# Optimization experiments

Measured on AMD Instinct MI355X. Metric: run time of the kernel, lower is better.

The kernel has to match this reference:

```python
import jax, jax.numpy as jnp
from jax import lax
import numpy as np

B = 512

def setup_inputs() -> dict:
    key = jax.random.key(0)
    ks = jax.random.split(key, 6)
    x = jax.random.normal(ks[0], (B, 1, 28, 28), jnp.float32)
    conv1_w = jax.random.normal(ks[1], (256, 1, 9, 9), jnp.float32) * 0.05
    conv1_b = jnp.zeros((256,), jnp.float32)
    prim_w = jax.random.normal(ks[2], (32, 32, 1, 9, 9), jnp.float32) * 0.02
    prim_b = jnp.zeros((32,), jnp.float32)
    dig_W = jax.random.normal(ks[3], (1152, 8, 16), jnp.float32) * 0.1
    dig_Wb = jnp.zeros((1152, 16), jnp.float32)
    out_w = jax.random.normal(ks[4], (10, 10, 16, 1), jnp.float32) * 0.1
    out_b = jnp.zeros((10,), jnp.float32)
    return dict(x=x, conv1_w=conv1_w, conv1_b=conv1_b, prim_w=prim_w, prim_b=prim_b,
                dig_W=dig_W, dig_Wb=dig_Wb, out_w=out_w, out_b=out_b)


def _squash(s):
    # s: [B, 16, 10]; matches torch: v = ||s||_2/(1+||s||_2) * (s^T / ||s||_1)
    l2 = jnp.sqrt(jnp.sum(s * s, axis=1))[:, :, None]      # [B, 10, 1]
    l1 = jnp.sum(jnp.abs(s), axis=1)[:, :, None]            # [B, 10, 1]
    return l2 / (1.0 + l2) * (jnp.swapaxes(s, 1, 2) / l1)   # [B, 10, 16]


def reference(x, conv1_w, conv1_b, prim_w, prim_b, dig_W, dig_Wb, out_w, out_b):
    # conv1: [B,1,28,28] -> [B,256,20,20]
    out = lax.conv_general_dilated(x, conv1_w, (1, 1), 'VALID',
                                   dimension_numbers=('NCHW', 'OIHW', 'NCHW'))
    out = jax.nn.relu(out + conv1_b[None, :, None, None])
    # primary capsules: [B,32,8,20,20] -> [B,32,8,6,6]
    out1 = out.reshape(-1, 32, 8, 20, 20)
    out1 = lax.conv_general_dilated(out1, prim_w, (1, 2, 2), 'VALID',
                                    dimension_numbers=('NCDHW', 'OIDHW', 'NCDHW'))
    out1 = jax.nn.relu(out1 + prim_b[None, :, None, None, None])
    # transpose(2,-1) then reshape -> [B, 1152, 8]
    u = jnp.swapaxes(out1, 2, 4).reshape(-1, 1152, 8)
    # per-capsule affine: [B,1152,16]
    dig = jnp.einsum('bnd,nde->bne', u, dig_W) + dig_Wb
    bsz = dig.shape[0]
    # dynamic routing: b logits are never updated in the source, so
    # c = softmax(zeros, dim=1) = 1/1152 uniform, and all 3 iterations produce
    # the identical v. Computed once (same math as the original loop).
    c = jnp.full((bsz, 1152, 10), 1.0 / 1152, dtype=dig.dtype)
    s = jnp.einsum('bni,bnd->bdi', c, dig)   # [B, 16, 10]
    v = _squash(s)                            # [B, 10, 16]
    # output Conv2d(10,10,[16,1]) on v[...,None] reduces fully -> [B,10]
    logits = jnp.einsum('bik,oik->bo', v, out_w[..., 0]) + out_b
    return jax.nn.softmax(logits, axis=1)
```

## Files before the change

### kernel.cpp

```cpp
#include <hip/hip_runtime.h>
#include <math.h>


typedef __attribute__((ext_vector_type(8))) short bf16x8;
typedef __attribute__((ext_vector_type(4))) float f32x4;

__device__ inline unsigned short f2bf(float f) {
    union { float f; unsigned u; } v; v.f = f;
    unsigned r = v.u + 0x7fff + ((v.u >> 16) & 1);
    return (unsigned short)(r >> 16);
}

#define C1TN 16008

__global__ void caps_pre(const float* __restrict__ conv1_w,
                         const float* __restrict__ prim_w,
                         const float* __restrict__ dig_Wb,
                         const float* __restrict__ out_w,
                         float* __restrict__ S,
                         float* __restrict__ colsum,
                         float* __restrict__ OW,
                         unsigned short* __restrict__ c1wp2,
                         unsigned short* __restrict__ pw2,
                         unsigned int* __restrict__ cnt,
                         int B)
{
    const int t = threadIdx.x;
    const int bx = blockIdx.x;

    if (bx < 32) {
        __shared__ float lw[2592];
        const float* src = prim_w + bx * 32 * 81;
        for (int j = t; j < 2592; j += 256) lw[j] = src[j];
        __syncthreads();
        unsigned short* dst = pw2 + bx * 32;
        for (int f = t; f < 2720; f += 256) {
            const int tap = f >> 5, s = f & 31;
            const int ci = (s >> 1) + ((s & 1) << 4);
            const unsigned short v =
                (tap < 81) ? f2bf(lw[ci * 81 + tap]) : (unsigned short)0;
            dst[tap * 1024 + s] = v;
        }
        return;
    }
    if (bx < 128) {
        const int tid = (bx - 32) * 256 + t;
        const int c = tid / 96, kn = tid % 96;
        unsigned short v = 0;
        if (kn < 72) {
            const int p = kn >> 1, lo = kn & 1, ky = p >> 2, kx = 2 * (p & 3) + lo;
            v = f2bf(conv1_w[c * 81 + 9 * ky + kx]);
        } else if (kn < 81) {
            v = f2bf(conv1_w[c * 81 + 9 * (kn - 72) + 8]);
        }
        c1wp2[tid] = v;
        return;
    }
    if (bx == 128) {
        __shared__ float cs[16];
        if (t < 16) cs[t] = 0.f;
        __syncthreads();
        {
            const int k = t & 15, g = t >> 4;
            float s = 0.f;
            for (int j = 0; j < 72; ++j) s += dig_Wb[(g * 72 + j) * 16 + k];
            atomicAdd(&cs[k], s);
        }
        __syncthreads();
        if (t < 16) colsum[t] = cs[t];
        if (t >= 64 && t < 224) {
            const int idx = t - 64, o = idx >> 4, k = idx & 15;
            float s = 0.f;
            for (int i = 0; i < 10; ++i) s += out_w[(o * 10 + i) * 16 + k];
            OW[idx] = s;
        }
        return;
    }
    const int idx = (bx - 129) * 256 + t;
    if (idx < B * 16) S[idx] = 0.f;
    else if (idx < B * 17) cnt[idx - B * 16] = 0u;
}

__global__ __launch_bounds__(256, 3) void caps_main(
    const float* __restrict__ x,
    const float* __restrict__ conv1_b,
    const float* __restrict__ prim_b,
    const float* __restrict__ dig_W,
    const unsigned short* __restrict__ c1wp2,
    const unsigned short* __restrict__ pw2,
    float* __restrict__ S,
    const float* __restrict__ colsum,
    const float* __restrict__ OW,
    const float* __restrict__ out_b,
    unsigned int* __restrict__ cnt,
    float* __restrict__ out)
{
    __shared__ __align__(16) unsigned short c1t[C1TN];
    __shared__ __align__(16) unsigned imgp[1120];
    __shared__ unsigned short offT[64];
    __shared__ float pbs[32];
    __shared__ float sacc[64];

    const int b = blockIdx.x >> 3, d = blockIdx.x & 7;
    const int t = threadIdx.x;
    const int wave = t >> 6, lane = t & 63, quad = lane >> 4, l16 = lane & 15;

    const int base = wave * 21;

    const unsigned short* apbase = pw2 + l16 * 32 + quad * 8;
    bf16x8 A0a = *(const bf16x8*)(apbase + (base + 0) * 1024);
    bf16x8 A0b = *(const bf16x8*)(apbase + (base + 0) * 1024 + 512);
    bf16x8 A1a = *(const bf16x8*)(apbase + (base + 1) * 1024);
    bf16x8 A1b = *(const bf16x8*)(apbase + (base + 1) * 1024 + 512);
    bf16x8 A2a = *(const bf16x8*)(apbase + (base + 2) * 1024);
    bf16x8 A2b = *(const bf16x8*)(apbase + (base + 2) * 1024 + 512);
    bf16x8 Bw0[3], Bw1[3];
#pragma unroll
    for (int ks = 0; ks < 3; ++ks) {
        Bw0[ks] = *(const bf16x8*)&c1wp2[(l16 * 8 + d) * 96 + ks * 32 + quad * 8];
        Bw1[ks] = *(const bf16x8*)&c1wp2[((16 + l16) * 8 + d) * 96 + ks * 32 + quad * 8];
    }
    const float cb0 = conv1_b[l16 * 8 + d];
    const float cb1 = conv1_b[(16 + l16) * 8 + d];
    __builtin_amdgcn_sched_barrier(0);

    const float* xb = x + b * 784;
    if (t < 196) {
        const float4 f4 = *(const float4*)(xb + 4 * t);
        const float nxt = (t < 195) ? xb[4 * t + 4] : 0.f;
        const float e[5] = {f4.x, f4.y, f4.z, f4.w, nxt};
#pragma unroll
        for (int r = 0; r < 4; ++r) {
            const int j = 4 * t + r;
            const int y = (int)(((unsigned)j * 37450u) >> 20);
            const int xc = j - 28 * y;
            const float cnext = (xc < 27) ? e[r + 1] : 0.f;
            imgp[y * 40 + xc] = (unsigned)f2bf(e[r]) | ((unsigned)f2bf(cnext) << 16);
        }
    }
    for (int j = t; j < 1120; j += 256) {
        const int y = (int)(((unsigned)j * 1639u) >> 16);
        if (j - 40 * y >= 28) imgp[j] = 0u;
    }
    if (t < 64) {
        int v;
        if (t < 32) {
            const int ky = t >> 2, kx = 2 * (t & 3);
            v = ky * 40 + kx;
        } else {
            const int k = t + 32;
            if (k < 72) {
                const int p = k >> 1, lo = k & 1, ky = p >> 2, kx = 2 * (p & 3) + lo;
                v = ky * 40 + kx;
            } else if (k < 81) {
                v = (k - 72) * 40 + 8;
            } else v = 28;
        }
        offT[t] = (unsigned short)(4 * v);
    }
    if (t < 32) pbs[t] = prim_b[t];
    __syncthreads();

    unsigned tp0[4], tp1[4], t2a[4], t2b[4];
#pragma unroll
    for (int r = 0; r < 4; ++r) {
        tp0[r] = offT[quad * 4 + r];
        tp1[r] = offT[16 + quad * 4 + r];
        t2a[r] = offT[32 + quad * 8 + 2 * r];
        t2b[r] = offT[32 + quad * 8 + 2 * r + 1];
    }

    {
        for (int mt = wave; mt < 25; mt += 4) {
            const int pos = mt * 16 + l16;
            const int y = (int)(((unsigned)pos * 52429u) >> 20);
            const unsigned pb4 = (unsigned)(pos + 20 * y) * 4u;
            f32x4 a0 = {0.f, 0.f, 0.f, 0.f}, a1 = {0.f, 0.f, 0.f, 0.f};
            union { unsigned u[4]; bf16x8 v; } A;
#pragma unroll
            for (int r = 0; r < 4; ++r)
                A.u[r] = *(const unsigned*)((const char*)imgp + (pb4 + tp0[r]));
            a0 = __builtin_amdgcn_mfma_f32_16x16x32_bf16(A.v, Bw0[0], a0, 0, 0, 0);
            a1 = __builtin_amdgcn_mfma_f32_16x16x32_bf16(A.v, Bw1[0], a1, 0, 0, 0);
#pragma unroll
            for (int r = 0; r < 4; ++r)
                A.u[r] = *(const unsigned*)((const char*)imgp + (pb4 + tp1[r]));
            a0 = __builtin_amdgcn_mfma_f32_16x16x32_bf16(A.v, Bw0[1], a0, 0, 0, 0);
            a1 = __builtin_amdgcn_mfma_f32_16x16x32_bf16(A.v, Bw1[1], a1, 0, 0, 0);
#pragma unroll
            for (int r = 0; r < 4; ++r) {
                const unsigned lo = *(const unsigned*)((const char*)imgp + (pb4 + t2a[r]));
                const unsigned hi = *(const unsigned*)((const char*)imgp + (pb4 + t2b[r]));
                A.u[r] = (lo & 0xFFFFu) | (hi << 16);
            }
            a0 = __builtin_amdgcn_mfma_f32_16x16x32_bf16(A.v, Bw0[2], a0, 0, 0, 0);
            a1 = __builtin_amdgcn_mfma_f32_16x16x32_bf16(A.v, Bw1[2], a1, 0, 0, 0);
#pragma unroll
            for (int r = 0; r < 4; ++r) {
                const int pr = mt * 16 + quad * 4 + r;
                const int spar = (int)((((unsigned)pr * 52429u) >> 21) & 1u);
                const int base2 = pr * 40 + 8 * spar;
                const unsigned pk = (unsigned)f2bf(fmaxf(a0[r] + cb0, 0.f))
                                  | ((unsigned)f2bf(fmaxf(a1[r] + cb1, 0.f)) << 16);
                *(unsigned*)&c1t[base2 + 2 * l16] = pk;
            }
        }
    }
    __syncthreads();

    const int hp = l16 >> 3, wp = l16 & 7;
    const unsigned Lbase = 80u * (unsigned)(40 * hp + 2 * wp) + 16u * quad;
    const unsigned Lh0 = Lbase + 16u * hp;
    const unsigned Lh1 = Lbase + 16u * (1 - hp);

    f32x4 pa[6];
#pragma unroll
    for (int q = 0; q < 6; ++q) pa[q] = (f32x4){0.f, 0.f, 0.f, 0.f};

    bf16x8 P0a = *(const bf16x8*)(apbase + (base + 3) * 1024);
    bf16x8 P0b = *(const bf16x8*)(apbase + (base + 3) * 1024 + 512);
    bf16x8 P1a = *(const bf16x8*)(apbase + (base + 4) * 1024);
    bf16x8 P1b = *(const bf16x8*)(apbase + (base + 4) * 1024 + 512);
    bf16x8 P2a = *(const bf16x8*)(apbase + (base + 5) * 1024);
    bf16x8 P2b = *(const bf16x8*)(apbase + (base + 5) * 1024 + 512);
    __builtin_amdgcn_sched_barrier(0);

#pragma unroll
    for (int g = 0; g < 7; ++g) {
        if (g < 6 || wave != 3) {
            int nb = base + 3 * g + 6;
            nb = (nb > 82) ? 82 : nb;
            const bf16x8 N0a = *(const bf16x8*)(apbase + (nb + 0) * 1024);
            const bf16x8 N0b = *(const bf16x8*)(apbase + (nb + 0) * 1024 + 512);
            const bf16x8 N1a = *(const bf16x8*)(apbase + (nb + 1) * 1024);
            const bf16x8 N1b = *(const bf16x8*)(apbase + (nb + 1) * 1024 + 512);
            const bf16x8 N2a = *(const bf16x8*)(apbase + (nb + 2) * 1024);
            const bf16x8 N2b = *(const bf16x8*)(apbase + (nb + 2) * 1024 + 512);
            __builtin_amdgcn_sched_barrier(0);

#pragma unroll
            for (int j = 0; j < 3; ++j) {
                const int off = base + 3 * g + j;
                const int ky = (off * 57) >> 9;
                const int kx = off - 9 * ky;
                const int kk = (ky >> 1) & 1;
                const unsigned soff = 80u * (unsigned)(20 * ky + kx);
                const unsigned ad = (kk ? Lh1 : Lh0) + soff;
                const char* b0 = (const char*)c1t + ad;
                const bf16x8 Aa = (j == 0) ? A0a : (j == 1) ? A1a : A2a;
                const bf16x8 Ab = (j == 0) ? A0b : (j == 1) ? A1b : A2b;
#pragma unroll
                for (int nt = 0; nt < 3; ++nt) {
                    const bf16x8 Bf = *(const bf16x8*)(b0 + nt * 6400);
                    pa[nt]     = __builtin_amdgcn_mfma_f32_16x16x32_bf16(Aa, Bf, pa[nt],     0, 0, 0);
                    pa[3 + nt] = __builtin_amdgcn_mfma_f32_16x16x32_bf16(Ab, Bf, pa[3 + nt], 0, 0, 0);
                }
            }
            A0a = P0a; A0b = P0b; A1a = P1a; A1b = P1b; A2a = P2a; A2b = P2b;
            P0a = N0a; P0b = N0b; P1a = N1a; P1b = N1b; P2a = N2a; P2b = N2b;
        }
    }
    __syncthreads();

    f32x4* redbuf = (f32x4*)c1t;
#pragma unroll
    for (int q = 0; q < 6; ++q) redbuf[(wave * 6 + q) * 64 + lane] = pa[q];
    __syncthreads();

    float part[16];
#pragma unroll
    for (int k = 0; k < 16; ++k) part[k] = 0.f;

#define FOLDQ(QV)                                                           \
    {                                                                       \
        const int q = (QV);                                                 \
        f32x4 u4 = redbuf[q * 64 + lane];                                   \
        u4 += redbuf[(6 + q) * 64 + lane];                                  \
        u4 += redbuf[(12 + q) * 64 + lane];                                 \
        u4 += redbuf[(18 + q) * 64 + lane];                                 \
        if (wp < 6) {                                                       \
            const int mt = (q >= 3) ? 1 : 0;                                \
            const int nt = q - 3 * mt;                                      \
            const int h = 2 * nt + hp;                                      \
            _Pragma("unroll")                                               \
            for (int r = 0; r < 4; ++r) {                                   \
                const int o = mt * 16 + quad * 4 + r;                       \
                const float val = fmaxf(u4[r] + pbs[o], 0.f);               \
                const int nc = o * 36 + wp * 6 + h;                         \
                const f32x4* wd = (const f32x4*)&dig_W[(nc * 8 + d) * 16];  \
                _Pragma("unroll")                                           \
                for (int m = 0; m < 4; ++m) {                               \
                    const f32x4 wv = wd[m];                                 \
                    part[m * 4 + 0] = fmaf(val, wv[0], part[m * 4 + 0]);    \
                    part[m * 4 + 1] = fmaf(val, wv[1], part[m * 4 + 1]);    \
                    part[m * 4 + 2] = fmaf(val, wv[2], part[m * 4 + 2]);    \
                    part[m * 4 + 3] = fmaf(val, wv[3], part[m * 4 + 3]);    \
                }                                                           \
            }                                                               \
        }                                                                   \
    }

    FOLDQ(wave);
    if (wave < 2) FOLDQ(wave + 4);
#undef FOLDQ

    float v8[8];
    {
        const bool hi5 = (lane & 32) != 0;
#pragma unroll
        for (int j = 0; j < 8; ++j) {
            const float keep = hi5 ? part[8 + j] : part[j];
            const float send = hi5 ? part[j] : part[8 + j];
            v8[j] = keep + __shfl_xor(send, 32, 64);
        }
    }
    float v4[4];
    {
        const bool hi4 = (lane & 16) != 0;
#pragma unroll
        for (int j = 0; j < 4; ++j) {
            const float keep = hi4 ? v8[4 + j] : v8[j];
            const float send = hi4 ? v8[j] : v8[4 + j];
            v4[j] = keep + __shfl_xor(send, 16, 64);
        }
    }
    float v2[2];
    {
        const bool hi3 = (lane & 8) != 0;
#pragma unroll
        for (int j = 0; j < 2; ++j) {
            const float keep = hi3 ? v4[2 + j] : v4[j];
            const float send = hi3 ? v4[j] : v4[2 + j];
            v2[j] = keep + __shfl_xor(send, 8, 64);
        }
    }
    float v1;
    {
        const bool hi2 = (lane & 4) != 0;
        const float keep = hi2 ? v2[1] : v2[0];
        const float send = hi2 ? v2[0] : v2[1];
        v1 = keep + __shfl_xor(send, 4, 64);
    }
    v1 += __shfl_xor(v1, 2, 64);
    v1 += __shfl_xor(v1, 1, 64);
    if ((lane & 3) == 0) sacc[wave * 16 + ((lane >> 2) & 15)] = v1;
    __syncthreads();
    if (t < 16) {
        const float v = sacc[t] + sacc[16 + t] + sacc[32 + t] + sacc[48 + t];
        atomicAdd(&S[b * 16 + t], v);
    }
    __syncthreads();

    if (t == 0) {
        const unsigned old = atomicAdd(&cnt[b], 1u);
        if (old == 7u) {
            float Sv[16]; float l2 = 0.f, l1 = 0.f;
#pragma unroll
            for (int k = 0; k < 16; ++k) {
                const float sv = (__hip_atomic_load(&S[b * 16 + k], __ATOMIC_RELAXED,
                                                    __HIP_MEMORY_SCOPE_AGENT)
                                  + colsum[k]) * (1.f / 1152.f);
                Sv[k] = sv; l2 += sv * sv; l1 += fabsf(sv);
            }
            l2 = sqrtf(l2);
            const float sc = l2 / (1.f + l2) / l1;
            float lg[10]; float mx = -1e30f;
#pragma unroll
            for (int o = 0; o < 10; ++o) {
                float a = out_b[o];
#pragma unroll
                for (int k = 0; k < 16; ++k) a = fmaf(Sv[k] * sc, OW[o * 16 + k], a);
                lg[o] = a; mx = fmaxf(mx, a);
            }
            float sum = 0.f;
#pragma unroll
            for (int o = 0; o < 10; ++o) { lg[o] = expf(lg[o] - mx); sum += lg[o]; }
            const float inv = 1.f / sum;
#pragma unroll
            for (int o = 0; o < 10; ++o) out[b * 10 + o] = lg[o] * inv;
        }
    }
}

extern "C" void kernel_launch(void* const* d_in, const int* in_sizes, int n_in,
                              void* d_out, int out_size, void* d_ws, size_t ws_size,
                              hipStream_t stream) {
    const float* x       = (const float*)d_in[0];
    const float* conv1_w = (const float*)d_in[1];
    const float* conv1_b = (const float*)d_in[2];
    const float* prim_w  = (const float*)d_in[3];
    const float* prim_b  = (const float*)d_in[4];
    const float* dig_W   = (const float*)d_in[5];
    const float* dig_Wb  = (const float*)d_in[6];
    const float* out_w   = (const float*)d_in[7];
    const float* out_b   = (const float*)d_in[8];
    float* out = (float*)d_out;

    const int B = in_sizes[0] / 784;

    char* w = (char*)d_ws;
    float* S              = (float*)(w);
    float* colsum         = (float*)(w + 32768);
    float* OW             = (float*)(w + 32832);
    unsigned short* c1wp2 = (unsigned short*)(w + 33472);
    unsigned short* pw2   = (unsigned short*)(w + 33472 + 49152);
    unsigned int* cnt     = (unsigned int*)(w + 256704);

    const int zblocks = (B * 17 + 255) / 256;
    caps_pre<<<129 + zblocks, 256, 0, stream>>>(conv1_w, prim_w, dig_Wb, out_w,
                                                S, colsum, OW, c1wp2, pw2, cnt, B);
    caps_main<<<B * 8, 256, 0, stream>>>(x, conv1_b, prim_b, dig_W, c1wp2, pw2,
                                         S, colsum, OW, out_b, cnt, out);
}
```

Before: 167.7 us.

## Stream primary-capsule weights through LDS via async global_load_lds ring buffer

```diff
diff --git a/kernel.cpp b/kernel.cpp
--- a/kernel.cpp
+++ b/kernel.cpp
@@ -9,6 +9,13 @@
     union { float f; unsigned u; } v; v.f = f;
     unsigned r = v.u + 0x7fff + ((v.u >> 16) & 1);
     return (unsigned short)(r >> 16);
+}
+
+__device__ inline void gload16(const unsigned short* g, unsigned short* l) {
+    __builtin_amdgcn_global_load_lds(
+        (const __attribute__((address_space(1))) void*)g,
+        (__attribute__((address_space(3))) void*)l,
+        16, 0, 0);
 }
 
 #define C1TN 16008
@@ -81,7 +88,7 @@
     else if (idx < B * 17) cnt[idx - B * 16] = 0u;
 }
 
-__global__ __launch_bounds__(256, 3) void caps_main(
+__global__ __launch_bounds__(256, 2) void caps_main(
     const float* __restrict__ x,
     const float* __restrict__ conv1_b,
     const float* __restrict__ prim_b,
@@ -96,6 +103,7 @@
     float* __restrict__ out)
 {
     __shared__ __align__(16) unsigned short c1t[C1TN];
+    __shared__ __align__(16) unsigned short abuf[4][4][1024];
     __shared__ __align__(16) unsigned imgp[1120];
     __shared__ unsigned short offT[64];
     __shared__ float pbs[32];
@@ -106,14 +114,15 @@
     const int wave = t >> 6, lane = t & 63, quad = lane >> 4, l16 = lane & 15;
 
     const int base = wave * 21;
-
-    const unsigned short* apbase = pw2 + l16 * 32 + quad * 8;
-    bf16x8 A0a = *(const bf16x8*)(apbase + (base + 0) * 1024);
-    bf16x8 A0b = *(const bf16x8*)(apbase + (base + 0) * 1024 + 512);
-    bf16x8 A1a = *(const bf16x8*)(apbase + (base + 1) * 1024);
-    bf16x8 A1b = *(const bf16x8*)(apbase + (base + 1) * 1024 + 512);
-    bf16x8 A2a = *(const bf16x8*)(apbase + (base + 2) * 1024);
-    bf16x8 A2b = *(const bf16x8*)(apbase + (base + 2) * 1024 + 512);
+    const int ntap = (wave == 3) ? 18 : 21;
+
+#pragma unroll
+    for (int p = 0; p < 3; ++p) {
+        const unsigned short* g = pw2 + (base + p) * 1024 + lane * 8;
+        unsigned short* l = &abuf[wave][p][0];
+        gload16(g, l);
+        gload16(g + 512, l + 512);
+    }
     bf16x8 Bw0[3], Bw1[3];
 #pragma unroll
     for (int ks = 0; ks < 3; ++ks) {
@@ -217,47 +226,32 @@
 #pragma unroll
     for (int q = 0; q < 6; ++q) pa[q] = (f32x4){0.f, 0.f, 0.f, 0.f};
 
-    bf16x8 P0a = *(const bf16x8*)(apbase + (base + 3) * 1024);
-    bf16x8 P0b = *(const bf16x8*)(apbase + (base + 3) * 1024 + 512);
-    bf16x8 P1a = *(const bf16x8*)(apbase + (base + 4) * 1024);
-    bf16x8 P1b = *(const bf16x8*)(apbase + (base + 4) * 1024 + 512);
-    bf16x8 P2a = *(const bf16x8*)(apbase + (base + 5) * 1024);
-    bf16x8 P2b = *(const bf16x8*)(apbase + (base + 5) * 1024 + 512);
-    __builtin_amdgcn_sched_barrier(0);
-
-#pragma unroll
-    for (int g = 0; g < 7; ++g) {
-        if (g < 6 || wave != 3) {
-            int nb = base + 3 * g + 6;
-            nb = (nb > 82) ? 82 : nb;
-            const bf16x8 N0a = *(const bf16x8*)(apbase + (nb + 0) * 1024);
-            const bf16x8 N0b = *(const bf16x8*)(apbase + (nb + 0) * 1024 + 512);
-            const bf16x8 N1a = *(const bf16x8*)(apbase + (nb + 1) * 1024);
-            const bf16x8 N1b = *(const bf16x8*)(apbase + (nb + 1) * 1024 + 512);
-            const bf16x8 N2a = *(const bf16x8*)(apbase + (nb + 2) * 1024);
-            const bf16x8 N2b = *(const bf16x8*)(apbase + (nb + 2) * 1024 + 512);
-            __builtin_amdgcn_sched_barrier(0);
-
-#pragma unroll
-            for (int j = 0; j < 3; ++j) {
-                const int off = base + 3 * g + j;
-                const int ky = (off * 57) >> 9;
-                const int kx = off - 9 * ky;
-                const int kk = (ky >> 1) & 1;
-                const unsigned soff = 80u * (unsigned)(20 * ky + kx);
-                const unsigned ad = (kk ? Lh1 : Lh0) + soff;
-                const char* b0 = (const char*)c1t + ad;
-                const bf16x8 Aa = (j == 0) ? A0a : (j == 1) ? A1a : A2a;
-                const bf16x8 Ab = (j == 0) ? A0b : (j == 1) ? A1b : A2b;
-#pragma unroll
-                for (int nt = 0; nt < 3; ++nt) {
-                    const bf16x8 Bf = *(const bf16x8*)(b0 + nt * 6400);
-                    pa[nt]     = __builtin_amdgcn_mfma_f32_16x16x32_bf16(Aa, Bf, pa[nt],     0, 0, 0);
-                    pa[3 + nt] = __builtin_amdgcn_mfma_f32_16x16x32_bf16(Ab, Bf, pa[3 + nt], 0, 0, 0);
-                }
-            }
-            A0a = P0a; A0b = P0b; A1a = P1a; A1b = P1b; A2a = P2a; A2b = P2b;
-            P0a = N0a; P0b = N0b; P1a = N1a; P1b = N1b; P2a = N2a; P2b = N2b;
+    for (int k = 0; k < ntap; ++k) {
+        const int nk = k + 3;
+        if (nk < ntap) {
+            const unsigned short* g = pw2 + (base + nk) * 1024 + lane * 8;
+            unsigned short* l = &abuf[wave][nk & 3][0];
+            gload16(g, l);
+            gload16(g + 512, l + 512);
+        }
+        asm volatile("s_waitcnt vmcnt(6)" ::: "memory");
+
+        const unsigned short* ab = &abuf[wave][k & 3][0];
+        const bf16x8 Aa = *(const bf16x8*)(ab + l16 * 32 + quad * 8);
+        const bf16x8 Ab = *(const bf16x8*)(ab + 512 + l16 * 32 + quad * 8);
+
+        const int off = base + k;
+        const int ky = (off * 57) >> 9;
+        const int kx = off - 9 * ky;
+        const int kk = (ky >> 1) & 1;
+        const unsigned soff = 80u * (unsigned)(20 * ky + kx);
+        const unsigned ad = (kk ? Lh1 : Lh0) + soff;
+        const char* b0 = (const char*)c1t + ad;
+#pragma unroll
+        for (int nt = 0; nt < 3; ++nt) {
+            const bf16x8 Bf = *(const bf16x8*)(b0 + nt * 6400);
+            pa[nt]     = __builtin_amdgcn_mfma_f32_16x16x32_bf16(Aa, Bf, pa[nt],     0, 0, 0);
+            pa[3 + nt] = __builtin_amdgcn_mfma_f32_16x16x32_bf16(Ab, Bf, pa[3 + nt], 0, 0, 0);
         }
     }
     __syncthreads();
```

New measurement: 208.6 us. 24.3% more time.
